# Kernel tuning notes

Measured on AMD Instinct MI355X. Metric: run time of the kernel, lower is better.

Reference implementation:

```python
import jax, jax.numpy as jnp
import numpy as np

N_NODES = 50000
N_EDGES = 800000
IN_FEATS = 96
H_FEATS = 256
N_HOPS = 3
N_NIE = N_HOPS + 1  # hops 0..3
NDIM_FC = N_NIE * H_FEATS


def setup_inputs() -> dict:
    key = jax.random.key(0)
    ks = jax.random.split(key, 8)
    edge_index = jax.random.randint(ks[0], (2, N_EDGES), 0, N_NODES, dtype=jnp.int64)
    features = jax.random.normal(ks[1], (N_NODES, IN_FEATS), dtype=jnp.float32)
    # per-hop MLP params: Linear(in_feats, h_feats) for each of n_nie hops
    s_in = 1.0 / np.sqrt(IN_FEATS)
    Ws = jax.random.uniform(ks[2], (N_NIE, IN_FEATS, H_FEATS), jnp.float32, -s_in, s_in)
    bs = jax.random.uniform(ks[3], (N_NIE, H_FEATS), jnp.float32, -s_in, s_in)
    # fusion: Linear(ndim_fc, h_feats)
    s_fc = 1.0 / np.sqrt(NDIM_FC)
    Wf = jax.random.uniform(ks[4], (NDIM_FC, H_FEATS), jnp.float32, -s_fc, s_fc)
    bf = jax.random.uniform(ks[5], (H_FEATS,), jnp.float32, -s_fc, s_fc)
    return {"edge_index": edge_index, "features": features, "Ws": Ws, "bs": bs, "Wf": Wf, "bf": bf}


def _build_norm_adj(edge_index):
    """set_diag (remove existing diag, add unit self-loops) + symmetric D^-1/2 A D^-1/2.
    Returns (rows, cols, edge_w) COO of the normalized adjacency."""
    row, col = edge_index[0].astype(jnp.int32), edge_index[1].astype(jnp.int32)
    loop = jnp.arange(N_NODES, dtype=jnp.int32)
    rows = jnp.concatenate([row, loop])
    cols = jnp.concatenate([col, loop])
    # zero out any pre-existing diagonal entries, self-loops get weight 1 (set_diag semantics)
    w = jnp.concatenate([(row != col).astype(jnp.float32), jnp.ones((N_NODES,), jnp.float32)])
    deg = jax.ops.segment_sum(w, rows, num_segments=N_NODES)
    dinv = jnp.where(deg > 0, jax.lax.rsqrt(deg), 0.0)
    edge_w = dinv[rows] * w * dinv[cols]
    return rows, cols, edge_w


def _spmm(rows, cols, edge_w, x):
    # out[r] = sum_e w_e * x[cols[e]] for edges with rows[e]==r
    return jax.ops.segment_sum(edge_w[:, None] * x[cols], rows, num_segments=N_NODES)


def reference(edge_index, features, Ws, bs, Wf, bf):
    rows, cols, edge_w = _build_norm_adj(edge_index)
    # row-normalize features (F.normalize dim=1)
    x = features / jnp.maximum(jnp.linalg.norm(features, axis=1, keepdims=True), 1e-12)
    nei_feats = [x]
    h = x
    for _ in range(N_HOPS):
        h = _spmm(rows, cols, edge_w, h)
        nei_feats.append(h)
    # per-hop MLP (dropout p=0 -> identity; norm=None -> identity) then ReLU
    ns = [jax.nn.relu(nei_feats[i] @ Ws[i] + bs[i]) for i in range(N_NIE)]
    cat = jnp.concatenate(ns, axis=1)  # [N, ndim_fc]
    out = jax.nn.relu(cat @ Wf + bf)   # [N, h_feats]
    return out
```

## Files before the change

kernel.cpp:

```cpp
#include <hip/hip_runtime.h>

#define N_NODES 50000
#define N_EDGES 800000
#define IN_F 96
#define H_F 256
#define N_NIE 4
#define SCAN_NB 196
#define BM 64
#define NBLK 782
#define LDA1 104
#define LDW 40

typedef float f32x4 __attribute__((ext_vector_type(4)));
typedef short s16x8 __attribute__((ext_vector_type(8)));
typedef unsigned short ushort;

__device__ __forceinline__ ushort bf16_rne(float f) {
    unsigned u = __float_as_uint(f);
    u += 0x7fffu + ((u >> 16) & 1u);
    return (ushort)(u >> 16);
}
__device__ __forceinline__ float bf16_f(ushort h) {
    return __uint_as_float(((unsigned)h) << 16);
}

__global__ __launch_bounds__(256) void k_count(const int* __restrict__ rows,
                                               const int* __restrict__ cols,
                                               int* __restrict__ cnt) {
    int i = blockIdx.x * 256 + threadIdx.x;
    if (i >= N_EDGES / 2) return;
    int2 r2 = ((const int2*)rows)[i];
    int2 c2 = ((const int2*)cols)[i];
    if (r2.x != c2.x) atomicAdd(&cnt[r2.x], 1);
    if (r2.y != c2.y) atomicAdd(&cnt[r2.y], 1);
}

__global__ __launch_bounds__(256) void k_scan1(const int* __restrict__ cnt,
                                               int* __restrict__ rowptr,
                                               int* __restrict__ bsum) {
    __shared__ int s[256];
    int t = threadIdx.x, e = blockIdx.x * 256 + t;
    int v = (e < N_NODES) ? cnt[e] : 0;
    s[t] = v;
    __syncthreads();
    #pragma unroll
    for (int off = 1; off < 256; off <<= 1) {
        int nv = (t >= off) ? s[t - off] : 0;
        __syncthreads();
        s[t] += nv;
        __syncthreads();
    }
    if (e < N_NODES) rowptr[e] = s[t] - v;
    if (t == 255) bsum[blockIdx.x] = s[255];
}

__global__ __launch_bounds__(256) void k_scan2(int* __restrict__ bsum,
                                               int* __restrict__ boff,
                                               int* __restrict__ rowptr) {
    __shared__ int s[256];
    int t = threadIdx.x;
    int v = (t < SCAN_NB) ? bsum[t] : 0;
    s[t] = v;
    __syncthreads();
    #pragma unroll
    for (int off = 1; off < 256; off <<= 1) {
        int nv = (t >= off) ? s[t - off] : 0;
        __syncthreads();
        s[t] += nv;
        __syncthreads();
    }
    if (t < SCAN_NB) boff[t] = s[t] - v;
    if (t == 255) rowptr[N_NODES] = s[255];
}

__global__ __launch_bounds__(256) void k_scan3(const int* __restrict__ boff,
                                               const int* __restrict__ cnt,
                                               int* __restrict__ rowptr,
                                               int* __restrict__ cursor,
                                               float* __restrict__ dinv) {
    int e = blockIdx.x * 256 + threadIdx.x;
    if (e >= N_NODES) return;
    int r = rowptr[e] + boff[blockIdx.x];
    rowptr[e] = r;
    cursor[e] = r;
    dinv[e] = rsqrtf((float)cnt[e] + 1.0f);
}

__global__ __launch_bounds__(256) void k_scatter(const int* __restrict__ rows,
                                                 const int* __restrict__ cols,
                                                 const float* __restrict__ dinv,
                                                 int* __restrict__ cursor,
                                                 int2* __restrict__ cw) {
    int e = blockIdx.x * 256 + threadIdx.x;
    if (e >= N_EDGES) return;
    int r = rows[e], c = cols[e];
    if (r == c) return;
    int p = atomicAdd(&cursor[r], 1);
    long long v = ((long long)(unsigned)__float_as_int(dinv[c]) << 32) | (unsigned)c;
    __builtin_nontemporal_store(v, (long long*)&cw[p]);
}

__global__ __launch_bounds__(256) void k_wsplit(const float* __restrict__ src,
                                                ushort* __restrict__ dh,
                                                int K, int N, int total) {
    int idx = blockIdx.x * 256 + threadIdx.x;
    if (idx >= total) return;
    int kn = K * N;
    int g = idx / kn, rem = idx - g * kn;
    int k = rem / N, n = rem - k * N;
    dh[g * kn + n * K + k] = bf16_rne(src[idx]);
}

__global__ __launch_bounds__(256) void k_norm(const float* __restrict__ feat,
                                              ushort* __restrict__ x) {
    int wid = (blockIdx.x * 256 + threadIdx.x) >> 6;
    int lane = threadIdx.x & 63;
    if (wid >= N_NODES) return;
    const float* fr = feat + (size_t)wid * IN_F;
    float v0 = (lane < IN_F) ? fr[lane] : 0.0f;
    float v1 = (lane < IN_F - 64) ? fr[64 + lane] : 0.0f;
    float ss = v0 * v0 + v1 * v1;
    #pragma unroll
    for (int o = 32; o; o >>= 1) ss += __shfl_xor(ss, o, 64);
    float inv = 1.0f / fmaxf(sqrtf(ss), 1e-12f);
    ushort* xr = x + (size_t)wid * IN_F;
    if (lane < IN_F) xr[lane] = bf16_rne(v0 * inv);
    if (lane < IN_F - 64) xr[64 + lane] = bf16_rne(v1 * inv);
}

__global__ __launch_bounds__(256) void k_spmm_csr(const int* __restrict__ rowptr,
                                                  const int2* __restrict__ cw,
                                                  const float* __restrict__ dinv,
                                                  const ushort* __restrict__ x,
                                                  ushort* __restrict__ y) {
    int g = (blockIdx.x * 256 + threadIdx.x) >> 5;
    if (g >= N_NODES) return;
    int l = threadIdx.x & 31;
    float dr = dinv[g];
    const ushort* xg = x + (size_t)g * IN_F;
    float s0 = bf16_f(xg[l]), s1 = bf16_f(xg[l + 32]), s2 = bf16_f(xg[l + 64]);
    float a0 = 0.f, a1 = 0.f, a2 = 0.f;
    float b0 = 0.f, b1 = 0.f, b2 = 0.f;
    float c0 = 0.f, c1 = 0.f, c2 = 0.f;
    float d0 = 0.f, d1 = 0.f, d2 = 0.f;
    int k = rowptr[g], e = rowptr[g + 1];
    for (; k + 3 < e; k += 4) {
        int2 p0 = cw[k], p1 = cw[k + 1], p2 = cw[k + 2], p3 = cw[k + 3];
        const ushort* x0 = x + (size_t)p0.x * IN_F;
        const ushort* x1 = x + (size_t)p1.x * IN_F;
        const ushort* x2 = x + (size_t)p2.x * IN_F;
        const ushort* x3 = x + (size_t)p3.x * IN_F;
        float w0 = __int_as_float(p0.y), w1 = __int_as_float(p1.y);
        float w2 = __int_as_float(p2.y), w3 = __int_as_float(p3.y);
        a0 += bf16_f(x0[l]) * w0; a1 += bf16_f(x0[l + 32]) * w0; a2 += bf16_f(x0[l + 64]) * w0;
        b0 += bf16_f(x1[l]) * w1; b1 += bf16_f(x1[l + 32]) * w1; b2 += bf16_f(x1[l + 64]) * w1;
        c0 += bf16_f(x2[l]) * w2; c1 += bf16_f(x2[l + 32]) * w2; c2 += bf16_f(x2[l + 64]) * w2;
        d0 += bf16_f(x3[l]) * w3; d1 += bf16_f(x3[l + 32]) * w3; d2 += bf16_f(x3[l + 64]) * w3;
    }
    for (; k < e; ++k) {
        int2 p0 = cw[k];
        float w0 = __int_as_float(p0.y);
        const ushort* x0 = x + (size_t)p0.x * IN_F;
        a0 += bf16_f(x0[l]) * w0; a1 += bf16_f(x0[l + 32]) * w0; a2 += bf16_f(x0[l + 64]) * w0;
    }
    ushort* yr = y + (size_t)g * IN_F;
    yr[l]      = bf16_rne(dr * ((a0 + b0) + (c0 + d0) + dr * s0));
    yr[l + 32] = bf16_rne(dr * ((a1 + b1) + (c1 + d1) + dr * s1));
    yr[l + 64] = bf16_rne(dr * ((a2 + b2) + (c2 + d2) + dr * s2));
}

__global__ __launch_bounds__(512, 4) void k_mega(const ushort* __restrict__ h0,
                                                 const ushort* __restrict__ h1,
                                                 const ushort* __restrict__ h2,
                                                 const ushort* __restrict__ h3,
                                                 const ushort* __restrict__ WsT,
                                                 const float* __restrict__ bs,
                                                 const ushort* __restrict__ WfT,
                                                 const float* __restrict__ bf,
                                                 float* __restrict__ out) {
    __shared__ ushort SM[36864];
    ushort* nsH = SM;
    ushort* Wb0 = SM + 16384;
    ushort* Wb1 = SM + 26624;
    ushort* Bs = Wb0;
    ushort* Ah = Wb1;

    int m0 = blockIdx.x * BM;
    int tid = threadIdx.x;
    int lane = tid & 63, w = tid >> 6;
    int rsel = lane & 15, g = lane >> 4, ksel = g * 8;
    int crow = g * 4, ccol = rsel;
    int rw0 = (w & 3) * 16;
    int cwb = (w >> 2) * 32;

    f32x4 acc[4][2] = {};

    for (int hop = 0; hop < N_NIE; ++hop) {
        const ushort* A = (hop == 0) ? h0 : (hop == 1) ? h1 : (hop == 2) ? h2 : h3;
        const ushort* wsT = WsT + hop * IN_F * H_F;
        const ushort* wfT = WfT + hop * H_F * H_F;
        const float* bsi = bs + hop * H_F;

        #pragma unroll
        for (int p = 0; p < 2; ++p) {
            int flat = tid + p * 512;
            if (flat < 768) {
                int r = flat / 12, j = flat - r * 12;
                int gm = m0 + r;
                s16x8 v = {0, 0, 0, 0, 0, 0, 0, 0};
                if (gm < N_NODES) v = *(const s16x8*)&A[(size_t)gm * IN_F + j * 8];
                *(s16x8*)&Ah[r * LDA1 + j * 8] = v;
            }
        }
        #pragma unroll
        for (int c = 0; c < 4; ++c) {
            __syncthreads();
            #pragma unroll
            for (int p = 0; p < 2; ++p) {
                int flat = tid + p * 512;
                if (flat < 768) {
                    int r = flat / 12, j = flat - r * 12;
                    *(s16x8*)&Bs[r * LDA1 + j * 8] =
                        *(const s16x8*)&wsT[(size_t)(c * 64 + r) * IN_F + j * 8];
                }
            }
            __syncthreads();
            f32x4 ac[2] = {};
            #pragma unroll
            for (int ks = 0; ks < 3; ++ks) {
                int k0 = ks * 32 + ksel;
                s16x8 ah = *(const s16x8*)&Ah[(rw0 + rsel) * LDA1 + k0];
                s16x8 b0 = *(const s16x8*)&Bs[(cwb + rsel) * LDA1 + k0];
                s16x8 b1 = *(const s16x8*)&Bs[(cwb + 16 + rsel) * LDA1 + k0];
                ac[0] = __builtin_amdgcn_mfma_f32_16x16x32_bf16(ah, b0, ac[0], 0, 0, 0);
                ac[1] = __builtin_amdgcn_mfma_f32_16x16x32_bf16(ah, b1, ac[1], 0, 0, 0);
            }
            #pragma unroll
            for (int cf = 0; cf < 2; ++cf) {
                int col = c * 64 + cwb + cf * 16 + ccol;
                float bb = bsi[col];
                #pragma unroll
                for (int ii = 0; ii < 4; ++ii) {
                    int row = rw0 + crow + ii;
                    nsH[row * 256 + (col ^ ((row & 7) << 3))] =
                        bf16_rne(fmaxf(ac[cf][ii] + bb, 0.f));
                }
            }
        }
        s16x8 wreg[2];
        #pragma unroll
        for (int p = 0; p < 2; ++p) {
            int flat = tid + p * 512;
            int r = flat >> 2, j = flat & 3;
            wreg[p] = *(const s16x8*)&wfT[(size_t)r * H_F + j * 8];
        }
        __syncthreads();
        int cur = 0;
        #pragma unroll
        for (int kc = 0; kc < 8; ++kc) {
            ushort* Wcur = cur ? Wb1 : Wb0;
            #pragma unroll
            for (int p = 0; p < 2; ++p) {
                int flat = tid + p * 512;
                int r = flat >> 2, j = flat & 3;
                *(s16x8*)&Wcur[r * LDW + j * 8] = wreg[p];
            }
            __syncthreads();
            if (kc < 7) {
                #pragma unroll
                for (int p = 0; p < 2; ++p) {
                    int flat = tid + p * 512;
                    int r = flat >> 2, j = flat & 3;
                    wreg[p] = *(const s16x8*)&wfT[(size_t)r * H_F + (kc + 1) * 32 + j * 8];
                }
            }
            int k0 = kc * 32 + ksel;
            s16x8 ah4[4];
            #pragma unroll
            for (int rf = 0; rf < 4; ++rf) {
                int row = rf * 16 + rsel;
                ah4[rf] = *(const s16x8*)&nsH[row * 256 + (k0 ^ ((row & 7) << 3))];
            }
            #pragma unroll
            for (int cf = 0; cf < 2; ++cf) {
                s16x8 bh = *(const s16x8*)&Wcur[(w * 32 + cf * 16 + rsel) * LDW + ksel];
                #pragma unroll
                for (int rf = 0; rf < 4; ++rf)
                    acc[rf][cf] = __builtin_amdgcn_mfma_f32_16x16x32_bf16(ah4[rf], bh, acc[rf][cf], 0, 0, 0);
            }
            cur ^= 1;
        }
        __syncthreads();
    }
    #pragma unroll
    for (int cf = 0; cf < 2; ++cf) {
        int col = w * 32 + cf * 16 + ccol;
        float bb = bf[col];
        #pragma unroll
        for (int rf = 0; rf < 4; ++rf)
            #pragma unroll
            for (int ii = 0; ii < 4; ++ii) {
                int gm = m0 + rf * 16 + crow + ii;
                if (gm < N_NODES)
                    out[(size_t)gm * H_F + col] = fmaxf(acc[rf][cf][ii] + bb, 0.f);
            }
    }
}

extern "C" void kernel_launch(void* const* d_in, const int* in_sizes, int n_in,
                              void* d_out, int out_size, void* d_ws, size_t ws_size,
                              hipStream_t stream) {
    const int* ei = (const int*)d_in[0];
    const int* rows = ei;
    const int* cols = ei + N_EDGES;
    const float* feat = (const float*)d_in[1];
    const float* Ws = (const float*)d_in[2];
    const float* bs = (const float*)d_in[3];
    const float* Wf = (const float*)d_in[4];
    const float* bf = (const float*)d_in[5];
    float* out = (float*)d_out;

    ushort* h0 = (ushort*)d_ws;
    ushort* h1 = h0 + (size_t)N_NODES * IN_F;
    ushort* h2 = h1 + (size_t)N_NODES * IN_F;
    ushort* h3 = h2 + (size_t)N_NODES * IN_F;
    ushort* WsT = h3 + (size_t)N_NODES * IN_F;
    ushort* WfT = WsT + N_NIE * IN_F * H_F;
    float* dinv = (float*)(WfT + N_NIE * H_F * H_F);
    int* rowptr = (int*)(dinv + N_NODES);
    int* bsum = rowptr + 50004;
    int* boff = bsum + 256;
    int2* cw = (int2*)(boff + 256);
    int* cnt = (int*)h1;
    int* cursor = cnt + N_NODES;

    hipMemsetAsync(cnt, 0, N_NODES * sizeof(int), stream);
    k_count<<<(N_EDGES / 2 + 255) / 256, 256, 0, stream>>>(rows, cols, cnt);
    k_scan1<<<SCAN_NB, 256, 0, stream>>>(cnt, rowptr, bsum);
    k_scan2<<<1, 256, 0, stream>>>(bsum, boff, rowptr);
    k_scan3<<<SCAN_NB, 256, 0, stream>>>(boff, cnt, rowptr, cursor, dinv);
    k_scatter<<<(N_EDGES + 255) / 256, 256, 0, stream>>>(rows, cols, dinv, cursor, cw);
    k_wsplit<<<(N_NIE * IN_F * H_F + 255) / 256, 256, 0, stream>>>(Ws, WsT, IN_F, H_F,
                                                                   N_NIE * IN_F * H_F);
    k_wsplit<<<(N_NIE * H_F * H_F + 255) / 256, 256, 0, stream>>>(Wf, WfT, H_F, H_F,
                                                                  N_NIE * H_F * H_F);
    k_norm<<<(N_NODES + 3) / 4, 256, 0, stream>>>(feat, h0);

    k_spmm_csr<<<(N_NODES * 32 + 255) / 256, 256, 0, stream>>>(rowptr, cw, dinv, h0, h1);
    k_spmm_csr<<<(N_NODES * 32 + 255) / 256, 256, 0, stream>>>(rowptr, cw, dinv, h1, h2);
    k_spmm_csr<<<(N_NODES * 32 + 255) / 256, 256, 0, stream>>>(rowptr, cw, dinv, h2, h3);
    k_mega<<<NBLK, 512, 0, stream>>>(h0, h1, h2, h3, WsT, bs, WfT, bf, out);
}
```

Measured before the change: 320.0 us.

## Prefetch weight chunks into registers and stage output through LDS for coalesced stores

Prefetches the per-hop Ws chunks and the first two Wf chunks into registers one step ahead, so global loads overlap the MFMA work instead of sitting on the critical path. The Wf loop is unrolled by two with explicit ping-pong buffers, and the index math is hoisted out of the hop loop. The final epilogue transposes the accumulators through shared memory so the output is written as coalesced float4 stores. The cost is higher register pressure and extra barriers in the epilogue.

```diff
diff --git a/kernel.cpp b/kernel.cpp
--- a/kernel.cpp
+++ b/kernel.cpp
@@ -184,6 +184,7 @@
     ushort* Wb1 = SM + 26624;
     ushort* Bs = Wb0;
     ushort* Ah = Wb1;
+    float* T = (float*)SM;
 
     int m0 = blockIdx.x * BM;
     int tid = threadIdx.x;
@@ -193,6 +194,11 @@
     int rw0 = (w & 3) * 16;
     int cwb = (w >> 2) * 32;
 
+    int sr0 = tid / 12, sj0 = tid - sr0 * 12;
+    int f1 = tid + 512;
+    int sr1 = f1 / 12, sj1 = f1 - sr1 * 12;
+    int wr_ = tid >> 2, wj_ = tid & 3;
+
     f32x4 acc[4][2] = {};
 
     for (int hop = 0; hop < N_NIE; ++hop) {
@@ -201,30 +207,41 @@
         const ushort* wfT = WfT + hop * H_F * H_F;
         const float* bsi = bs + hop * H_F;
 
-        #pragma unroll
-        for (int p = 0; p < 2; ++p) {
-            int flat = tid + p * 512;
-            if (flat < 768) {
-                int r = flat / 12, j = flat - r * 12;
-                int gm = m0 + r;
-                s16x8 v = {0, 0, 0, 0, 0, 0, 0, 0};
-                if (gm < N_NODES) v = *(const s16x8*)&A[(size_t)gm * IN_F + j * 8];
-                *(s16x8*)&Ah[r * LDA1 + j * 8] = v;
+        {
+            int gm = m0 + sr0;
+            s16x8 v = {0, 0, 0, 0, 0, 0, 0, 0};
+            if (gm < N_NODES) v = *(const s16x8*)&A[(size_t)gm * IN_F + sj0 * 8];
+            *(s16x8*)&Ah[sr0 * LDA1 + sj0 * 8] = v;
+            if (tid < 256) {
+                int gm1 = m0 + sr1;
+                s16x8 v1 = {0, 0, 0, 0, 0, 0, 0, 0};
+                if (gm1 < N_NODES) v1 = *(const s16x8*)&A[(size_t)gm1 * IN_F + sj1 * 8];
+                *(s16x8*)&Ah[sr1 * LDA1 + sj1 * 8] = v1;
             }
         }
+        s16x8 breg0 = *(const s16x8*)&wsT[(size_t)sr0 * IN_F + sj0 * 8];
+        s16x8 breg1 = {0, 0, 0, 0, 0, 0, 0, 0};
+        if (tid < 256) breg1 = *(const s16x8*)&wsT[(size_t)sr1 * IN_F + sj1 * 8];
+        s16x8 wrA[2], wrB[2];
         #pragma unroll
         for (int c = 0; c < 4; ++c) {
             __syncthreads();
-            #pragma unroll
-            for (int p = 0; p < 2; ++p) {
-                int flat = tid + p * 512;
-                if (flat < 768) {
-                    int r = flat / 12, j = flat - r * 12;
-                    *(s16x8*)&Bs[r * LDA1 + j * 8] =
-                        *(const s16x8*)&wsT[(size_t)(c * 64 + r) * IN_F + j * 8];
-                }
-            }
+            *(s16x8*)&Bs[sr0 * LDA1 + sj0 * 8] = breg0;
+            if (tid < 256) *(s16x8*)&Bs[sr1 * LDA1 + sj1 * 8] = breg1;
             __syncthreads();
+            if (c < 3) {
+                const ushort* src = wsT + (size_t)(c + 1) * 64 * IN_F;
+                breg0 = *(const s16x8*)&src[(size_t)sr0 * IN_F + sj0 * 8];
+                if (tid < 256) breg1 = *(const s16x8*)&src[(size_t)sr1 * IN_F + sj1 * 8];
+            } else {
+                #pragma unroll
+                for (int p = 0; p < 2; ++p) {
+                    wrA[p] = *(const s16x8*)&wfT[(size_t)((tid + p * 512) >> 2) * H_F +
+                                                 ((tid + p * 512) & 3) * 8];
+                    wrB[p] = *(const s16x8*)&wfT[(size_t)((tid + p * 512) >> 2) * H_F + 32 +
+                                                 ((tid + p * 512) & 3) * 8];
+                }
+            }
             f32x4 ac[2] = {};
             #pragma unroll
             for (int ks = 0; ks < 3; ++ks) {
@@ -247,63 +264,93 @@
                 }
             }
         }
-        s16x8 wreg[2];
+        __syncthreads();
         #pragma unroll
-        for (int p = 0; p < 2; ++p) {
-            int flat = tid + p * 512;
-            int r = flat >> 2, j = flat & 3;
-            wreg[p] = *(const s16x8*)&wfT[(size_t)r * H_F + j * 8];
+        for (int kc2 = 0; kc2 < 4; ++kc2) {
+            *(s16x8*)&Wb0[wr_ * LDW + wj_ * 8] = wrA[0];
+            *(s16x8*)&Wb0[(wr_ + 128) * LDW + wj_ * 8] = wrA[1];
+            __syncthreads();
+            if (kc2 < 3) {
+                #pragma unroll
+                for (int p = 0; p < 2; ++p)
+                    wrA[p] = *(const s16x8*)&wfT[(size_t)((tid + p * 512) >> 2) * H_F +
+                                                 (2 * kc2 + 2) * 32 +
+                                                 ((tid + p * 512) & 3) * 8];
+            }
+            {
+                int k0 = (2 * kc2) * 32 + ksel;
+                s16x8 ah4[4];
+                #pragma unroll
+                for (int rf = 0; rf < 4; ++rf) {
+                    int row = rf * 16 + rsel;
+                    ah4[rf] = *(const s16x8*)&nsH[row * 256 + (k0 ^ ((row & 7) << 3))];
+                }
+                #pragma unroll
+                for (int cf = 0; cf < 2; ++cf) {
+                    s16x8 bh = *(const s16x8*)&Wb0[(w * 32 + cf * 16 + rsel) * LDW + ksel];
+                    #pragma unroll
+                    for (int rf = 0; rf < 4; ++rf)
+                        acc[rf][cf] = __builtin_amdgcn_mfma_f32_16x16x32_bf16(ah4[rf], bh, acc[rf][cf], 0, 0, 0);
+                }
+            }
+            *(s16x8*)&Wb1[wr_ * LDW + wj_ * 8] = wrB[0];
+            *(s16x8*)&Wb1[(wr_ + 128) * LDW + wj_ * 8] = wrB[1];
+            __syncthreads();
+            if (kc2 < 3) {
+                #pragma unroll
+                for (int p = 0; p < 2; ++p)
+                    wrB[p] = *(const s16x8*)&wfT[(size_t)((tid + p * 512) >> 2) * H_F +
+                                                 (2 * kc2 + 3) * 32 +
+                                                 ((tid + p * 512) & 3) * 8];
+            }
+            {
+                int k0 = (2 * kc2 + 1) * 32 + ksel;
+                s16x8 ah4[4];
+                #pragma unroll
+                for (int rf = 0; rf < 4; ++rf) {
+                    int row = rf * 16 + rsel;
+                    ah4[rf] = *(const s16x8*)&nsH[row * 256 + (k0 ^ ((row & 7) << 3))];
+                }
+                #pragma unroll
+                for (int cf = 0; cf < 2; ++cf) {
+                    s16x8 bh = *(const s16x8*)&Wb1[(w * 32 + cf * 16 + rsel) * LDW + ksel];
+                    #pragma unroll
+                    for (int rf = 0; rf < 4; ++rf)
+                        acc[rf][cf] = __builtin_amdgcn_mfma_f32_16x16x32_bf16(ah4[rf], bh, acc[rf][cf], 0, 0, 0);
+                }
+            }
+            __syncthreads();
         }
-        __syncthreads();
-        int cur = 0;
+    }
+    #pragma unroll
+    for (int half = 0; half < 2; ++half) {
+        __syncthreads();
         #pragma unroll
-        for (int kc = 0; kc < 8; ++kc) {
-            ushort* Wcur = cur ? Wb1 : Wb0;
-            #pragma unroll
-            for (int p = 0; p < 2; ++p) {
-                int flat = tid + p * 512;
-                int r = flat >> 2, j = flat & 3;
-                *(s16x8*)&Wcur[r * LDW + j * 8] = wreg[p];
-            }
-            __syncthreads();
-            if (kc < 7) {
-                #pragma unroll
-                for (int p = 0; p < 2; ++p) {
-                    int flat = tid + p * 512;
-                    int r = flat >> 2, j = flat & 3;
-                    wreg[p] = *(const s16x8*)&wfT[(size_t)r * H_F + (kc + 1) * 32 + j * 8];
-                }
-            }
-            int k0 = kc * 32 + ksel;
-            s16x8 ah4[4];
-            #pragma unroll
-            for (int rf = 0; rf < 4; ++rf) {
-                int row = rf * 16 + rsel;
-                ah4[rf] = *(const s16x8*)&nsH[row * 256 + (k0 ^ ((row & 7) << 3))];
-            }
+        for (int rf2 = 0; rf2 < 2; ++rf2) {
+            int rf = half * 2 + rf2;
             #pragma unroll
             for (int cf = 0; cf < 2; ++cf) {
-                s16x8 bh = *(const s16x8*)&Wcur[(w * 32 + cf * 16 + rsel) * LDW + ksel];
-                #pragma unroll
-                for (int rf = 0; rf < 4; ++rf)
-                    acc[rf][cf] = __builtin_amdgcn_mfma_f32_16x16x32_bf16(ah4[rf], bh, acc[rf][cf], 0, 0, 0);
-            }
-            cur ^= 1;
+                int col = w * 32 + cf * 16 + ccol;
+                #pragma unroll
+                for (int ii = 0; ii < 4; ++ii)
+                    T[(rf2 * 16 + crow + ii) * 260 + col] = acc[rf][cf][ii];
+            }
         }
         __syncthreads();
-    }
-    #pragma unroll
-    for (int cf = 0; cf < 2; ++cf) {
-        int col = w * 32 + cf * 16 + ccol;
-        float bb = bf[col];
         #pragma unroll
-        for (int rf = 0; rf < 4; ++rf)
-            #pragma unroll
-            for (int ii = 0; ii < 4; ++ii) {
-                int gm = m0 + rf * 16 + crow + ii;
-                if (gm < N_NODES)
-                    out[(size_t)gm * H_F + col] = fmaxf(acc[rf][cf][ii] + bb, 0.f);
-            }
+        for (int p = 0; p < 4; ++p) {
+            int flat = tid + p * 512;
+            int r = flat >> 6, jc = flat & 63;
+            int gm = m0 + half * 32 + r;
+            if (gm < N_NODES) {
+                f32x4 v = *(f32x4*)&T[r * 260 + jc * 4];
+                f32x4 bb = *(const f32x4*)&bf[jc * 4];
+                f32x4 o;
+                #pragma unroll
+                for (int q = 0; q < 4; ++q) o[q] = fmaxf(v[q] + bb[q], 0.f);
+                *(f32x4*)&out[(size_t)gm * H_F + jc * 4] = o;
+            }
+        }
     }
 }
 
```

Measured after the change: 300.9 us. 1.06x faster.
